# Kernel optimization log

Hardware: AMD Instinct MI355X
Metric: run time of the kernel (lower is better)

The kernel has to match this reference:

```python
import jax, jax.numpy as jnp
import numpy as np

B, T, NX, NY, E, BS = 2, 8, 32, 32, 768, 64
NB = E // BS            # 12 blocks
YM = NY // 2 + 1        # 17 rfft y modes
KM = 12                 # kept_modes (hardcoded in source)
XS = slice(YM - KM, YM + KM)  # slice(5,29) on the x-mode axis (faithful quirk: bounds use y_modes)
LAM = 0.01


def _ln(x, g, b, eps=1e-5):
    m = x.mean(-1, keepdims=True)
    v = ((x - m) ** 2).mean(-1, keepdims=True)
    return (x - m) / jnp.sqrt(v + eps) * g + b


def _softshrink(x, lam=LAM):
    return jnp.where(x > lam, x - lam, jnp.where(x < -lam, x + lam, jnp.zeros((), x.dtype)))


def setup_inputs() -> dict:
    key = jax.random.key(0)
    ks = jax.random.split(key, 8)
    s = 0.02
    return {
        'input': jax.random.normal(ks[0], (B, T, NX * NY, E), jnp.float32),
        'w1': s * jax.random.normal(ks[1], (2, NB, BS, BS), jnp.float32),
        'b1': s * jax.random.normal(ks[2], (2, 1, 1, 1, NB, BS), jnp.float32),
        'w2': s * jax.random.normal(ks[3], (2, NB, BS, BS), jnp.float32),
        'b2': s * jax.random.normal(ks[4], (2, 1, 1, 1, NB, BS), jnp.float32),
        'ln1_g': jnp.ones((E,), jnp.float32),
        'ln1_b': jnp.zeros((E,), jnp.float32),
        'ln2_g': jnp.ones((E,), jnp.float32),
        'ln2_b': jnp.zeros((E,), jnp.float32),
        'mw1': s * jax.random.normal(ks[5], (E, 4 * E), jnp.float32),
        'mb1': jnp.zeros((4 * E,), jnp.float32),
        'mw2': s * jax.random.normal(ks[6], (4 * E, E), jnp.float32),
        'mb2': jnp.zeros((E,), jnp.float32),
    }


def reference(input, w1, b1, w2, b2, ln1_g, ln1_b, ln2_g, ln2_b, mw1, mb1, mw2, mb2):
    residual = input
    h = _ln(input, ln1_g, ln1_b)                       # ln1
    r = h.reshape(B, T, NX, NY, E)
    fc = jnp.fft.rfft2(r, axes=(2, 3), norm='ortho')   # (B,T,NX,YM,E) complex
    fc = fc.reshape(B, T, NX, YM, NB, BS)
    fr = fc.real[:, :, XS, :KM]                        # (B,T,24,12,NB,BS)
    fi = fc.imag[:, :, XS, :KM]
    op = 'btxyni,nio->btxyno'
    o1r = jax.nn.gelu(jnp.einsum(op, fr, w1[0]) - jnp.einsum(op, fi, w1[1]) + b1[0], approximate=False)
    o1i = jax.nn.gelu(jnp.einsum(op, fi, w1[0]) + jnp.einsum(op, fr, w1[1]) + b1[1], approximate=False)
    o2r = jnp.einsum(op, o1r, w2[0]) - jnp.einsum(op, o1i, w2[1]) + b2[0]
    o2i = jnp.einsum(op, o1i, w2[0]) + jnp.einsum(op, o1r, w2[1]) + b2[1]
    out_r = jnp.zeros(fc.shape, jnp.float32).at[:, :, XS, :KM].set(_softshrink(o2r))
    out_i = jnp.zeros(fc.shape, jnp.float32).at[:, :, XS, :KM].set(_softshrink(o2i))
    oc = (out_r + 1j * out_i).reshape(B, T, NX, YM, E)
    spat = jnp.fft.irfft2(oc, s=(NX, NY), axes=(2, 3), norm='ortho').reshape(B, T, NX * NY, E)
    out = spat + h + residual                          # faithful: adds ln1(input) and original input
    res2 = out
    out = _ln(out, ln2_g, ln2_b)                       # ln2
    out = jax.nn.gelu(out @ mw1 + mb1, approximate=False) @ mw2 + mb2
    return out + res2
```

## Files before the change

kernel.cpp:

```cpp
#include <hip/hip_runtime.h>
#include <hip/hip_bf16.h>
#include <math.h>

typedef __bf16 bf16;
typedef __bf16 bf16x8 __attribute__((ext_vector_type(8)));
typedef float f32x4 __attribute__((ext_vector_type(4)));
typedef short short8 __attribute__((ext_vector_type(8)));

#define E_ 768
#define S_ 1024
#define BT_ 16
#define KM_ 12
#define KX_ 24
#define NPOS_ 4608
#define NB_ 12
#define TWOPI_32 0.19634954084936207740f

__device__ __forceinline__ float gelu_fast(float x) {
    float t = x * x;
    float u = x * fmaf(t, 0.0356774081f, 0.7978845608f);
    float e = __expf(2.0f * u);
    float th = fmaf(-2.0f, __fdividef(1.0f, e + 1.0f), 1.0f);
    float hx = 0.5f * x;
    return fmaf(hx, th, hx);
}

__device__ __forceinline__ bf16x8 neg8(bf16x8 v) {
    short8 s;
    __builtin_memcpy(&s, &v, 16);
    s ^= (short)0x8000;
    bf16x8 r;
    __builtin_memcpy(&r, &s, 16);
    return r;
}

__device__ __forceinline__ void gload16(bf16* lds, const bf16* g) {
    __builtin_amdgcn_global_load_lds(
        (const __attribute__((address_space(1))) void*)g,
        (__attribute__((address_space(3))) void*)lds,
        16, 0, 0);
}

__global__ __launch_bounds__(256) void k_ln_stats(const float* __restrict__ x,
                                                  float* __restrict__ mu, float* __restrict__ rs) {
    int w = threadIdx.x >> 6, l = threadIdx.x & 63;
    int row = blockIdx.x * 4 + w;
    const float4* p = (const float4*)(x + (size_t)row * E_ + l * 12);
    float4 a = p[0], b = p[1], c = p[2];
    float s  = a.x + a.y + a.z + a.w + b.x + b.y + b.z + b.w + c.x + c.y + c.z + c.w;
    float ss = a.x*a.x + a.y*a.y + a.z*a.z + a.w*a.w
             + b.x*b.x + b.y*b.y + b.z*b.z + b.w*b.w
             + c.x*c.x + c.y*c.y + c.z*c.z + c.w*c.w;
    #pragma unroll
    for (int off = 32; off > 0; off >>= 1) {
        s  += __shfl_xor(s, off);
        ss += __shfl_xor(ss, off);
    }
    if (l == 0) {
        float m = s * (1.0f / E_);
        float var = ss * (1.0f / E_) - m * m;
        mu[row] = m;
        rs[row] = rsqrtf(var + 1e-5f);
    }
}

__global__ __launch_bounds__(256) void k_ln2(const float* __restrict__ x,
                                             const float* __restrict__ g,
                                             const float* __restrict__ b,
                                             bf16* __restrict__ out) {
    int w = threadIdx.x >> 6, l = threadIdx.x & 63;
    int row = blockIdx.x * 4 + w;
    int e0 = l * 12;
    const float4* p = (const float4*)(x + (size_t)row * E_ + e0);
    float4 va = p[0], vb = p[1], vc = p[2];
    float v[12] = {va.x, va.y, va.z, va.w, vb.x, vb.y, vb.z, vb.w, vc.x, vc.y, vc.z, vc.w};
    float s = 0.f, ss = 0.f;
    #pragma unroll
    for (int j = 0; j < 12; j++) { s += v[j]; ss += v[j] * v[j]; }
    #pragma unroll
    for (int off = 32; off > 0; off >>= 1) {
        s  += __shfl_xor(s, off);
        ss += __shfl_xor(ss, off);
    }
    float m = s * (1.0f / E_);
    float var = ss * (1.0f / E_) - m * m;
    float r = rsqrtf(var + 1e-5f);
    const float4* gp = (const float4*)(g + e0);
    const float4* bp = (const float4*)(b + e0);
    float4 g0 = gp[0], g1 = gp[1], g2 = gp[2];
    float4 b0 = bp[0], b1 = bp[1], b2 = bp[2];
    float gg[12] = {g0.x, g0.y, g0.z, g0.w, g1.x, g1.y, g1.z, g1.w, g2.x, g2.y, g2.z, g2.w};
    float bbv[12] = {b0.x, b0.y, b0.z, b0.w, b1.x, b1.y, b1.z, b1.w, b2.x, b2.y, b2.z, b2.w};
    bf16 ov[12];
    #pragma unroll
    for (int j = 0; j < 12; j++) ov[j] = (bf16)((v[j] - m) * r * gg[j] + bbv[j]);
    bf16* op = out + (size_t)row * E_ + e0;
    *(uint2*)(op)     = *(uint2*)&ov[0];
    *(uint2*)(op + 4) = *(uint2*)&ov[4];
    *(uint2*)(op + 8) = *(uint2*)&ov[8];
}

__global__ __launch_bounds__(256) void k_dft_y(const float* __restrict__ inp,
                                               const float* __restrict__ mu, const float* __restrict__ rs,
                                               const float* __restrict__ g, const float* __restrict__ bb,
                                               float* __restrict__ gre, float* __restrict__ gim) {
    int bid = blockIdx.x;
    int ec = bid % 3, x = (bid / 3) % 32, bt = bid / 96;
    int t = threadIdx.x;
    int e = ec * 256 + t;
    float gv = g[e], bv = bb[e];
    int row0 = bt * S_ + x * 32;
    const float* base = inp + (size_t)row0 * E_ + e;
    float v[32];
    #pragma unroll
    for (int y = 0; y < 32; y++) {
        float m = mu[row0 + y], r = rs[row0 + y];
        v[y] = (base[(size_t)y * E_] - m) * r * gv + bv;
    }
    for (int ky = 0; ky < KM_; ky++) {
        float cK, sK;
        sincosf(TWOPI_32 * ky, &sK, &cK);
        float c = 1.f, s = 0.f, re = 0.f, ims = 0.f;
        #pragma unroll
        for (int y = 0; y < 32; y++) {
            re  = fmaf(v[y], c, re);
            ims = fmaf(v[y], s, ims);
            float cn = c * cK - s * sK;
            s = fmaf(s, cK, c * sK);
            c = cn;
        }
        size_t o = ((size_t)((bt * 32 + x) * KM_ + ky)) * E_ + e;
        gre[o] = re; gim[o] = -ims;
    }
}

__global__ __launch_bounds__(256) void k_dft_x(const float* __restrict__ gre, const float* __restrict__ gim,
                                               float* __restrict__ fr, float* __restrict__ fi) {
    int bid = blockIdx.x;
    int ec = bid % 3, ky = (bid / 3) % KM_, bt = bid / (3 * KM_);
    int t = threadIdx.x;
    int eo = ec * 256 + t;
    float gr[32], gi[32];
    #pragma unroll
    for (int x = 0; x < 32; x++) {
        size_t o = ((size_t)((bt * 32 + x) * KM_ + ky)) * E_ + eo;
        gr[x] = gre[o]; gi[x] = gim[o];
    }
    for (int kxi = 0; kxi < KX_; kxi++) {
        int kx = kxi + 5;
        float cK, sK;
        sincosf(TWOPI_32 * kx, &sK, &cK);
        float c = 1.f, s = 0.f, re = 0.f, im = 0.f;
        #pragma unroll
        for (int x = 0; x < 32; x++) {
            re = fmaf(gr[x], c, re);
            re = fmaf(gi[x], s, re);
            im = fmaf(gi[x], c, im);
            im = fmaf(-gr[x], s, im);
            float cn = c * cK - s * sK;
            s = fmaf(s, cK, c * sK);
            c = cn;
        }
        size_t p = (size_t)(bt * KX_ + kxi) * KM_ + ky;
        fr[p * E_ + eo] = re * (1.0f / 32.0f);
        fi[p * E_ + eo] = im * (1.0f / 32.0f);
    }
}

__global__ __launch_bounds__(256) void k_blockmlp(float* fr, float* fi,
                                                  const float* __restrict__ w1, const float* __restrict__ b1,
                                                  const float* __restrict__ w2, const float* __restrict__ b2) {
    int n = blockIdx.x / 36;
    int p0 = (blockIdx.x % 36) * 128;
    int t = threadIdx.x;
    __shared__ __align__(16) bf16 lXr[128 * 72];
    __shared__ __align__(16) bf16 lXi[128 * 72];
    __shared__ __align__(16) bf16 lW1a[64 * 72];
    __shared__ __align__(16) bf16 lW1b[64 * 72];
    __shared__ __align__(16) bf16 lW2a[64 * 72];
    __shared__ __align__(16) bf16 lW2b[64 * 72];

    {
        int o = t & 63, iq = t >> 6;
        const float* s1a = w1 + (size_t)n * 4096;
        const float* s1b = w1 + (size_t)(NB_ + n) * 4096;
        const float* s2a = w2 + (size_t)n * 4096;
        const float* s2b = w2 + (size_t)(NB_ + n) * 4096;
        #pragma unroll
        for (int ii = 0; ii < 16; ii++) {
            int i = iq * 16 + ii;
            lW1a[o * 72 + i] = (bf16)s1a[i * 64 + o];
            lW1b[o * 72 + i] = (bf16)s1b[i * 64 + o];
            lW2a[o * 72 + i] = (bf16)s2a[i * 64 + o];
            lW2b[o * 72 + i] = (bf16)s2b[i * 64 + o];
        }
    }
    {
        int ch4 = (t & 15) * 4, prow = t >> 4;
        #pragma unroll
        for (int rep = 0; rep < 8; rep++) {
            int p = rep * 16 + prow;
            size_t ga = (size_t)(p0 + p) * E_ + n * 64 + ch4;
            float4 vr = *(const float4*)&fr[ga];
            float4 vi = *(const float4*)&fi[ga];
            bf16 br[4] = {(bf16)vr.x, (bf16)vr.y, (bf16)vr.z, (bf16)vr.w};
            bf16 bi[4] = {(bf16)vi.x, (bf16)vi.y, (bf16)vi.z, (bf16)vi.w};
            *(uint2*)&lXr[p * 72 + ch4] = *(uint2*)br;
            *(uint2*)&lXi[p * 72 + ch4] = *(uint2*)bi;
        }
    }
    int w = t >> 6, l = t & 63, lr = l & 15, lq = l >> 4;
    float bias1r[4], bias1i[4], bias2r[4], bias2i[4];
    #pragma unroll
    for (int ni = 0; ni < 4; ni++) {
        int o = n * 64 + ni * 16 + lr;
        bias1r[ni] = b1[o]; bias1i[ni] = b1[NB_ * 64 + o];
        bias2r[ni] = b2[o]; bias2i[ni] = b2[NB_ * 64 + o];
    }
    __syncthreads();

    f32x4 a1r[2][4], a1i[2][4];
    #pragma unroll
    for (int mt = 0; mt < 2; mt++)
        #pragma unroll
        for (int ni = 0; ni < 4; ni++) { a1r[mt][ni] = (f32x4){0,0,0,0}; a1i[mt][ni] = (f32x4){0,0,0,0}; }
    #pragma unroll
    for (int ks = 0; ks < 2; ks++) {
        int k0 = ks * 32;
        bf16x8 xr[2], xi[2], xin[2];
        #pragma unroll
        for (int mt = 0; mt < 2; mt++) {
            int row = w * 32 + mt * 16 + lr;
            xr[mt]  = *(bf16x8*)&lXr[row * 72 + k0 + lq * 8];
            xi[mt]  = *(bf16x8*)&lXi[row * 72 + k0 + lq * 8];
            xin[mt] = neg8(xi[mt]);
        }
        #pragma unroll
        for (int ni = 0; ni < 4; ni++) {
            bf16x8 ba = *(bf16x8*)&lW1a[(ni * 16 + lr) * 72 + k0 + lq * 8];
            bf16x8 bb = *(bf16x8*)&lW1b[(ni * 16 + lr) * 72 + k0 + lq * 8];
            #pragma unroll
            for (int mt = 0; mt < 2; mt++) {
                a1r[mt][ni] = __builtin_amdgcn_mfma_f32_16x16x32_bf16(xr[mt],  ba, a1r[mt][ni], 0, 0, 0);
                a1r[mt][ni] = __builtin_amdgcn_mfma_f32_16x16x32_bf16(xin[mt], bb, a1r[mt][ni], 0, 0, 0);
                a1i[mt][ni] = __builtin_amdgcn_mfma_f32_16x16x32_bf16(xi[mt],  ba, a1i[mt][ni], 0, 0, 0);
                a1i[mt][ni] = __builtin_amdgcn_mfma_f32_16x16x32_bf16(xr[mt],  bb, a1i[mt][ni], 0, 0, 0);
            }
        }
    }
    #pragma unroll
    for (int mt = 0; mt < 2; mt++)
        #pragma unroll
        for (int ni = 0; ni < 4; ni++) {
            int o = ni * 16 + lr;
            #pragma unroll
            for (int r = 0; r < 4; r++) {
                int row = w * 32 + mt * 16 + lq * 4 + r;
                lXr[row * 72 + o] = (bf16)gelu_fast(a1r[mt][ni][r] + bias1r[ni]);
                lXi[row * 72 + o] = (bf16)gelu_fast(a1i[mt][ni][r] + bias1i[ni]);
            }
        }

    f32x4 a2r[2][4], a2i[2][4];
    #pragma unroll
    for (int mt = 0; mt < 2; mt++)
        #pragma unroll
        for (int ni = 0; ni < 4; ni++) { a2r[mt][ni] = (f32x4){0,0,0,0}; a2i[mt][ni] = (f32x4){0,0,0,0}; }
    #pragma unroll
    for (int ks = 0; ks < 2; ks++) {
        int k0 = ks * 32;
        bf16x8 xr[2], xi[2], xin[2];
        #pragma unroll
        for (int mt = 0; mt < 2; mt++) {
            int row = w * 32 + mt * 16 + lr;
            xr[mt]  = *(bf16x8*)&lXr[row * 72 + k0 + lq * 8];
            xi[mt]  = *(bf16x8*)&lXi[row * 72 + k0 + lq * 8];
            xin[mt] = neg8(xi[mt]);
        }
        #pragma unroll
        for (int ni = 0; ni < 4; ni++) {
            bf16x8 ba = *(bf16x8*)&lW2a[(ni * 16 + lr) * 72 + k0 + lq * 8];
            bf16x8 bb = *(bf16x8*)&lW2b[(ni * 16 + lr) * 72 + k0 + lq * 8];
            #pragma unroll
            for (int mt = 0; mt < 2; mt++) {
                a2r[mt][ni] = __builtin_amdgcn_mfma_f32_16x16x32_bf16(xr[mt],  ba, a2r[mt][ni], 0, 0, 0);
                a2r[mt][ni] = __builtin_amdgcn_mfma_f32_16x16x32_bf16(xin[mt], bb, a2r[mt][ni], 0, 0, 0);
                a2i[mt][ni] = __builtin_amdgcn_mfma_f32_16x16x32_bf16(xi[mt],  ba, a2i[mt][ni], 0, 0, 0);
                a2i[mt][ni] = __builtin_amdgcn_mfma_f32_16x16x32_bf16(xr[mt],  bb, a2i[mt][ni], 0, 0, 0);
            }
        }
    }
    #pragma unroll
    for (int mt = 0; mt < 2; mt++)
        #pragma unroll
        for (int ni = 0; ni < 4; ni++) {
            int o = ni * 16 + lr;
            #pragma unroll
            for (int r = 0; r < 4; r++) {
                int row = w * 32 + mt * 16 + lq * 4 + r;
                float vr = a2r[mt][ni][r] + bias2r[ni];
                float vi = a2i[mt][ni][r] + bias2i[ni];
                vr = (vr > 0.01f) ? vr - 0.01f : ((vr < -0.01f) ? vr + 0.01f : 0.0f);
                vi = (vi > 0.01f) ? vi - 0.01f : ((vi < -0.01f) ? vi + 0.01f : 0.0f);
                size_t ga = (size_t)(p0 + row) * E_ + n * 64 + o;
                fr[ga] = vr;
                fi[ga] = vi;
            }
        }
}

__global__ __launch_bounds__(256) void k_idft_x(const float* __restrict__ pr_, const float* __restrict__ pi_,
                                                float* __restrict__ zre, float* __restrict__ zim) {
    int bid = blockIdx.x;
    int ec = bid % 3, ky = (bid / 3) % KM_, bt = bid / (3 * KM_);
    int t = threadIdx.x;
    int eo = ec * 256 + t;
    float pr[KX_], pi[KX_];
    #pragma unroll
    for (int kxi = 0; kxi < KX_; kxi++) {
        size_t p = (size_t)(bt * KX_ + kxi) * KM_ + ky;
        pr[kxi] = pr_[p * E_ + eo];
        pi[kxi] = pi_[p * E_ + eo];
    }
    for (int x = 0; x < 32; x++) {
        float cX, sX, c, s;
        sincosf(TWOPI_32 * x, &sX, &cX);
        sincosf(TWOPI_32 * ((5 * x) & 31), &s, &c);
        float re = 0.f, im = 0.f;
        #pragma unroll
        for (int kxi = 0; kxi < KX_; kxi++) {
            re = fmaf(pr[kxi], c, re);
            re = fmaf(-pi[kxi], s, re);
            im = fmaf(pr[kxi], s, im);
            im = fmaf(pi[kxi], c, im);
            float cn = c * cX - s * sX;
            s = fmaf(s, cX, c * sX);
            c = cn;
        }
        size_t zo = ((size_t)((bt * 32 + x) * KM_ + ky)) * E_ + eo;
        zre[zo] = re; zim[zo] = im;
    }
}

__global__ __launch_bounds__(256) void k_idft_y_res(const float* __restrict__ zre, const float* __restrict__ zim,
                                                    const float* __restrict__ inp,
                                                    const float* __restrict__ mu, const float* __restrict__ rs,
                                                    const float* __restrict__ g, const float* __restrict__ bb,
                                                    float* __restrict__ out) {
    int bid = blockIdx.x;
    int ec = bid % 3, x = (bid / 3) % 32, bt = bid / 96;
    int t = threadIdx.x;
    int e = ec * 256 + t;
    float zr[KM_], zi[KM_];
    #pragma unroll
    for (int ky = 0; ky < KM_; ky++) {
        size_t zo = ((size_t)((bt * 32 + x) * KM_ + ky)) * E_ + e;
        zr[ky] = zre[zo];
        zi[ky] = zim[zo];
    }
    float gv = g[e], bv = bb[e];
    int row0 = bt * S_ + x * 32;
    for (int y = 0; y < 32; y++) {
        float cY, sY;
        sincosf(TWOPI_32 * y, &sY, &cY);
        float C = 2.f * cY, S = 2.f * sY;
        float v = zr[0];
        #pragma unroll
        for (int ky = 1; ky < KM_; ky++) {
            v = fmaf(zr[ky], C, v);
            v = fmaf(-zi[ky], S, v);
            float Cn = C * cY - S * sY;
            S = fmaf(S, cY, C * sY);
            C = Cn;
        }
        v *= (1.0f / 32.0f);
        size_t o = (size_t)(row0 + y) * E_ + e;
        float iv = inp[o];
        float m = mu[row0 + y], r = rs[row0 + y];
        out[o] = v + ((iv - m) * r * gv + bv) + iv;
    }
}

__global__ void k_transpose_cast(const float* __restrict__ src, bf16* __restrict__ dst, int R, int C) {
    __shared__ float tile[32][33];
    int c0 = blockIdx.x * 32, r0 = blockIdx.y * 32;
    int tx = threadIdx.x, ty = threadIdx.y;
    #pragma unroll
    for (int j = 0; j < 32; j += 8)
        tile[ty + j][tx] = src[(size_t)(r0 + ty + j) * C + c0 + tx];
    __syncthreads();
    #pragma unroll
    for (int j = 0; j < 32; j += 8)
        dst[(size_t)(c0 + ty + j) * R + r0 + tx] = (bf16)tile[tx][ty + j];
}

template<bool FUSE_GELU>
__global__ __launch_bounds__(512, 2) void k_gemm(const bf16* __restrict__ A, const bf16* __restrict__ Bt,
                                                 const float* __restrict__ bias, int M, int N, int K,
                                                 bf16* __restrict__ outb, float* __restrict__ outf) {
    __shared__ __align__(16) bf16 lA[2][256 * 64];
    __shared__ __align__(16) bf16 lB[2][256 * 64];
    int t = threadIdx.x;
    int m0 = blockIdx.x * 256, n0 = blockIdx.y * 256;
    int w = t >> 6, l = t & 63;
    int wm = (w >> 2) * 128, wn = (w & 3) * 64;
    int lr = l & 15, lq = l >> 4;
    int s0 = (lq ^ (lr & 7)) * 8;
    int s1 = s0 ^ 32;

    int sil  = w * 8 + (l >> 3);
    int gcol = ((l & 7) ^ ((l >> 3) & 7)) * 8;
    const bf16* pa = A  + (size_t)(m0 + sil) * K + gcol;
    const bf16* pb = Bt + (size_t)(n0 + sil) * K + gcol;
    int lofs = (w * 8) * 64;

    f32x4 acc[8][4];
    #pragma unroll
    for (int i = 0; i < 8; i++)
        #pragma unroll
        for (int j = 0; j < 4; j++)
            acc[i][j] = (f32x4){0.f, 0.f, 0.f, 0.f};

    int nk = K / 64;
#define STAGE_T(T, d) do { const size_t _ko = (size_t)(T) * 64;                  \
        gload16(&lA[d][lofs],            pa + _ko);                              \
        gload16(&lA[d][lofs + 4096],     pa + (size_t)64  * K + _ko);            \
        gload16(&lA[d][lofs + 8192],     pa + (size_t)128 * K + _ko);            \
        gload16(&lA[d][lofs + 12288],    pa + (size_t)192 * K + _ko);            \
        gload16(&lB[d][lofs],            pb + _ko);                              \
        gload16(&lB[d][lofs + 4096],     pb + (size_t)64  * K + _ko);            \
        gload16(&lB[d][lofs + 8192],     pb + (size_t)128 * K + _ko);            \
        gload16(&lB[d][lofs + 12288],    pb + (size_t)192 * K + _ko);            \
    } while (0)

    STAGE_T(0, 0);
    STAGE_T(1, 1);
    asm volatile("s_waitcnt vmcnt(8)" ::: "memory");
    __builtin_amdgcn_sched_barrier(0);
    __builtin_amdgcn_s_barrier();

    for (int kt = 0; kt < nk; kt++) {
        int d = kt & 1;
        bf16x8 a0[8], a1[8], b0[4], b1[4];
        #pragma unroll
        for (int ni = 0; ni < 4; ni++) {
            int ro = (wn + ni * 16 + lr) * 64;
            b0[ni] = *(bf16x8*)&lB[d][ro + s0];
            b1[ni] = *(bf16x8*)&lB[d][ro + s1];
        }
        #pragma unroll
        for (int mi = 0; mi < 8; mi++) {
            int ro = (wm + mi * 16 + lr) * 64;
            a0[mi] = *(bf16x8*)&lA[d][ro + s0];
            a1[mi] = *(bf16x8*)&lA[d][ro + s1];
        }
        __builtin_amdgcn_s_setprio(1);
        #pragma unroll
        for (int mi = 0; mi < 8; mi++)
            #pragma unroll
            for (int ni = 0; ni < 4; ni++)
                acc[mi][ni] = __builtin_amdgcn_mfma_f32_16x16x32_bf16(a0[mi], b0[ni], acc[mi][ni], 0, 0, 0);
        __builtin_amdgcn_s_setprio(0);
        asm volatile("s_waitcnt lgkmcnt(0)" ::: "memory");
        __builtin_amdgcn_sched_barrier(0);
        __builtin_amdgcn_s_barrier();

        if (kt + 2 < nk) STAGE_T(kt + 2, d);
        __builtin_amdgcn_s_setprio(1);
        #pragma unroll
        for (int mi = 0; mi < 8; mi++)
            #pragma unroll
            for (int ni = 0; ni < 4; ni++)
                acc[mi][ni] = __builtin_amdgcn_mfma_f32_16x16x32_bf16(a1[mi], b1[ni], acc[mi][ni], 0, 0, 0);
        __builtin_amdgcn_s_setprio(0);
        if (kt + 1 < nk) {
            if (kt + 2 < nk) asm volatile("s_waitcnt vmcnt(8)" ::: "memory");
            else             asm volatile("s_waitcnt vmcnt(0)" ::: "memory");
            __builtin_amdgcn_sched_barrier(0);
            __builtin_amdgcn_s_barrier();
        }
    }
#undef STAGE_T

    #pragma unroll
    for (int mi = 0; mi < 8; mi++) {
        #pragma unroll
        for (int ni = 0; ni < 4; ni++) {
            int col = n0 + wn + ni * 16 + lr;
            float bv = bias[col];
            #pragma unroll
            for (int r = 0; r < 4; r++) {
                int row = m0 + wm + mi * 16 + lq * 4 + r;
                float v = acc[mi][ni][r] + bv;
                if (FUSE_GELU) {
                    outb[(size_t)row * N + col] = (bf16)gelu_fast(v);
                } else {
                    size_t oo = (size_t)row * N + col;
                    outf[oo] = v + outf[oo];
                }
            }
        }
    }
}

extern "C" void kernel_launch(void* const* d_in, const int* in_sizes, int n_in,
                              void* d_out, int out_size, void* d_ws, size_t ws_size,
                              hipStream_t stream) {
    const float* input = (const float*)d_in[0];
    const float* w1    = (const float*)d_in[1];
    const float* b1    = (const float*)d_in[2];
    const float* w2    = (const float*)d_in[3];
    const float* b2    = (const float*)d_in[4];
    const float* ln1g  = (const float*)d_in[5];
    const float* ln1b  = (const float*)d_in[6];
    const float* ln2g  = (const float*)d_in[7];
    const float* ln2b  = (const float*)d_in[8];
    const float* mw1   = (const float*)d_in[9];
    const float* mb1   = (const float*)d_in[10];
    const float* mw2   = (const float*)d_in[11];
    const float* mb2   = (const float*)d_in[12];
    float* out = (float*)d_out;

    float* ws = (float*)d_ws;
    float* mu  = ws;
    float* rs  = ws + 16384;
    const size_t BASE = 32768;
    float* gre = ws + BASE;
    float* gim = gre + 4718592;
    float* fr  = ws + BASE + 2 * 4718592;
    float* fi  = fr + 3538944;
    bf16* lnA = (bf16*)(ws + BASE);
    bf16* w1T = (bf16*)(ws + BASE + 6291456);
    bf16* w2T = (bf16*)(ws + BASE + 7471104);
    bf16* mid = (bf16*)(ws + BASE + 8650752);

    const size_t fixed_fl = BASE + 6291456 + 1179648 + 1179648;
    size_t avail_fl = ws_size / 4;
    int nch;
    if      (avail_fl >= fixed_fl + 25165824) nch = 1;
    else if (avail_fl >= fixed_fl + 12582912) nch = 2;
    else                                      nch = 4;
    int MC = 16384 / nch;

    k_ln_stats<<<4096, 256, 0, stream>>>(input, mu, rs);
    k_dft_y<<<BT_ * 32 * 3, 256, 0, stream>>>(input, mu, rs, ln1g, ln1b, gre, gim);
    k_dft_x<<<BT_ * KM_ * 3, 256, 0, stream>>>(gre, gim, fr, fi);
    k_blockmlp<<<NB_ * 36, 256, 0, stream>>>(fr, fi, w1, b1, w2, b2);
    k_idft_x<<<BT_ * KM_ * 3, 256, 0, stream>>>(fr, fi, gre, gim);
    k_idft_y_res<<<BT_ * 32 * 3, 256, 0, stream>>>(gre, gim, input, mu, rs, ln1g, ln1b, out);
    k_ln2<<<4096, 256, 0, stream>>>(out, ln2g, ln2b, lnA);
    k_transpose_cast<<<dim3(3072 / 32, 768 / 32), dim3(32, 8), 0, stream>>>(mw1, w1T, 768, 3072);
    k_transpose_cast<<<dim3(768 / 32, 3072 / 32), dim3(32, 8), 0, stream>>>(mw2, w2T, 3072, 768);
    for (int c = 0; c < nch; c++) {
        const bf16* aC = lnA + (size_t)c * MC * 768;
        float* oC = out + (size_t)c * MC * 768;
        k_gemm<true><<<dim3(MC / 256, 12), 512, 0, stream>>>(aC, w1T, mb1, MC, 3072, 768, mid, nullptr);
        k_gemm<false><<<dim3(MC / 256, 3), 512, 0, stream>>>(mid, w2T, mb2, MC, 768, 3072, nullptr, oC);
    }
}
```

Before: 497.4 us.

## Restructure GEMM main loop into four-phase half-K pipeline with split LDS layout

Splits each 64-wide K tile in shared memory into two 32-wide halves with a new XOR swizzle. The main loop becomes four quarter phases, each reading a smaller set of A/B fragments and issuing one half-tile global prefetch between barriers. This interleaves global loads, LDS reads and MFMA work more finely and lowers the number of live fragment registers. In exchange it adds more barriers per iteration and relies on intricate vmcnt bookkeeping, so a mistake in the load ordering could cause hazards.

```diff
diff --git a/kernel.cpp b/kernel.cpp
--- a/kernel.cpp
+++ b/kernel.cpp
@@ -398,21 +398,21 @@
 __global__ __launch_bounds__(512, 2) void k_gemm(const bf16* __restrict__ A, const bf16* __restrict__ Bt,
                                                  const float* __restrict__ bias, int M, int N, int K,
                                                  bf16* __restrict__ outb, float* __restrict__ outf) {
-    __shared__ __align__(16) bf16 lA[2][256 * 64];
-    __shared__ __align__(16) bf16 lB[2][256 * 64];
+    __shared__ __align__(16) bf16 lA[2][2][256][32];
+    __shared__ __align__(16) bf16 lB[2][2][256][32];
     int t = threadIdx.x;
     int m0 = blockIdx.x * 256, n0 = blockIdx.y * 256;
     int w = t >> 6, l = t & 63;
     int wm = (w >> 2) * 128, wn = (w & 3) * 64;
     int lr = l & 15, lq = l >> 4;
-    int s0 = (lq ^ (lr & 7)) * 8;
-    int s1 = s0 ^ 32;
-
-    int sil  = w * 8 + (l >> 3);
-    int gcol = ((l & 7) ^ ((l >> 3) & 7)) * 8;
-    const bf16* pa = A  + (size_t)(m0 + sil) * K + gcol;
-    const bf16* pb = Bt + (size_t)(n0 + sil) * K + gcol;
-    int lofs = (w * 8) * 64;
+    int ps = (lq ^ (lr & 3)) * 8;
+
+    int srow = l >> 2;
+    int gsw  = (((l & 3) ^ ((l >> 2) & 3)) * 8);
+    const bf16* pa0 = A  + (size_t)(m0 + w * 16 + srow) * K + gsw;
+    const bf16* pa1 = pa0 + (size_t)128 * K;
+    const bf16* pb0 = Bt + (size_t)(n0 + w * 16 + srow) * K + gsw;
+    const bf16* pb1 = pb0 + (size_t)128 * K;
 
     f32x4 acc[8][4];
     #pragma unroll
@@ -422,65 +422,109 @@
             acc[i][j] = (f32x4){0.f, 0.f, 0.f, 0.f};
 
     int nk = K / 64;
-#define STAGE_T(T, d) do { const size_t _ko = (size_t)(T) * 64;                  \
-        gload16(&lA[d][lofs],            pa + _ko);                              \
-        gload16(&lA[d][lofs + 4096],     pa + (size_t)64  * K + _ko);            \
-        gload16(&lA[d][lofs + 8192],     pa + (size_t)128 * K + _ko);            \
-        gload16(&lA[d][lofs + 12288],    pa + (size_t)192 * K + _ko);            \
-        gload16(&lB[d][lofs],            pb + _ko);                              \
-        gload16(&lB[d][lofs + 4096],     pb + (size_t)64  * K + _ko);            \
-        gload16(&lB[d][lofs + 8192],     pb + (size_t)128 * K + _ko);            \
-        gload16(&lB[d][lofs + 12288],    pb + (size_t)192 * K + _ko);            \
-    } while (0)
-
-    STAGE_T(0, 0);
-    STAGE_T(1, 1);
-    asm volatile("s_waitcnt vmcnt(8)" ::: "memory");
+#define ST_A(T, ks, db) do { size_t _c = (size_t)(T) * 64 + (ks) * 32;   \
+        gload16(&lA[db][ks][w * 16][0],       pa0 + _c);                 \
+        gload16(&lA[db][ks][128 + w * 16][0], pa1 + _c); } while (0)
+#define ST_B(T, ks, db) do { size_t _c = (size_t)(T) * 64 + (ks) * 32;   \
+        gload16(&lB[db][ks][w * 16][0],       pb0 + _c);                 \
+        gload16(&lB[db][ks][128 + w * 16][0], pb1 + _c); } while (0)
+
+    ST_A(0, 0, 0); ST_B(0, 0, 0); ST_A(0, 1, 0); ST_B(0, 1, 0);
+    if (nk > 1) {
+        ST_B(1, 0, 1); ST_A(1, 0, 1); ST_B(1, 1, 1);
+        asm volatile("s_waitcnt vmcnt(6)" ::: "memory");
+    } else {
+        asm volatile("s_waitcnt vmcnt(0)" ::: "memory");
+    }
     __builtin_amdgcn_sched_barrier(0);
     __builtin_amdgcn_s_barrier();
-
+    __builtin_amdgcn_sched_barrier(0);
+
+    bf16x8 bA[4], bB[4];
     for (int kt = 0; kt < nk; kt++) {
         int d = kt & 1;
-        bf16x8 a0[8], a1[8], b0[4], b1[4];
-        #pragma unroll
-        for (int ni = 0; ni < 4; ni++) {
-            int ro = (wn + ni * 16 + lr) * 64;
-            b0[ni] = *(bf16x8*)&lB[d][ro + s0];
-            b1[ni] = *(bf16x8*)&lB[d][ro + s1];
-        }
-        #pragma unroll
-        for (int mi = 0; mi < 8; mi++) {
-            int ro = (wm + mi * 16 + lr) * 64;
-            a0[mi] = *(bf16x8*)&lA[d][ro + s0];
-            a1[mi] = *(bf16x8*)&lA[d][ro + s1];
-        }
-        __builtin_amdgcn_s_setprio(1);
-        #pragma unroll
-        for (int mi = 0; mi < 8; mi++)
-            #pragma unroll
-            for (int ni = 0; ni < 4; ni++)
-                acc[mi][ni] = __builtin_amdgcn_mfma_f32_16x16x32_bf16(a0[mi], b0[ni], acc[mi][ni], 0, 0, 0);
-        __builtin_amdgcn_s_setprio(0);
-        asm volatile("s_waitcnt lgkmcnt(0)" ::: "memory");
-        __builtin_amdgcn_sched_barrier(0);
-        __builtin_amdgcn_s_barrier();
-
-        if (kt + 2 < nk) STAGE_T(kt + 2, d);
-        __builtin_amdgcn_s_setprio(1);
-        #pragma unroll
-        for (int mi = 0; mi < 8; mi++)
-            #pragma unroll
-            for (int ni = 0; ni < 4; ni++)
-                acc[mi][ni] = __builtin_amdgcn_mfma_f32_16x16x32_bf16(a1[mi], b1[ni], acc[mi][ni], 0, 0, 0);
-        __builtin_amdgcn_s_setprio(0);
-        if (kt + 1 < nk) {
-            if (kt + 2 < nk) asm volatile("s_waitcnt vmcnt(8)" ::: "memory");
+        {
+            bf16x8 a[4];
+            #pragma unroll
+            for (int ni = 0; ni < 4; ni++) bA[ni] = *(bf16x8*)&lB[d][0][wn + ni * 16 + lr][ps];
+            #pragma unroll
+            for (int mi = 0; mi < 4; mi++) a[mi] = *(bf16x8*)&lA[d][0][wm + mi * 16 + lr][ps];
+            if (kt + 1 < nk) ST_A(kt + 1, 1, d ^ 1);
+            __builtin_amdgcn_s_barrier();
+            asm volatile("s_waitcnt lgkmcnt(0)" ::: "memory");
+            __builtin_amdgcn_sched_barrier(0);
+            __builtin_amdgcn_s_setprio(1);
+            #pragma unroll
+            for (int mi = 0; mi < 4; mi++)
+                #pragma unroll
+                for (int ni = 0; ni < 4; ni++)
+                    acc[mi][ni] = __builtin_amdgcn_mfma_f32_16x16x32_bf16(a[mi], bA[ni], acc[mi][ni], 0, 0, 0);
+            __builtin_amdgcn_s_setprio(0);
+            __builtin_amdgcn_s_barrier();
+            __builtin_amdgcn_sched_barrier(0);
+        }
+        {
+            bf16x8 a[4];
+            #pragma unroll
+            for (int ni = 0; ni < 4; ni++) bB[ni] = *(bf16x8*)&lB[d][1][wn + ni * 16 + lr][ps];
+            #pragma unroll
+            for (int mi = 0; mi < 4; mi++) a[mi] = *(bf16x8*)&lA[d][0][wm + 64 + mi * 16 + lr][ps];
+            if (kt + 2 < nk) ST_B(kt + 2, 0, d);
+            __builtin_amdgcn_s_barrier();
+            asm volatile("s_waitcnt lgkmcnt(0)" ::: "memory");
+            __builtin_amdgcn_sched_barrier(0);
+            __builtin_amdgcn_s_setprio(1);
+            #pragma unroll
+            for (int mi = 0; mi < 4; mi++)
+                #pragma unroll
+                for (int ni = 0; ni < 4; ni++)
+                    acc[4 + mi][ni] = __builtin_amdgcn_mfma_f32_16x16x32_bf16(a[mi], bA[ni], acc[4 + mi][ni], 0, 0, 0);
+            __builtin_amdgcn_s_setprio(0);
+            __builtin_amdgcn_s_barrier();
+            __builtin_amdgcn_sched_barrier(0);
+        }
+        {
+            bf16x8 a[4];
+            #pragma unroll
+            for (int mi = 0; mi < 4; mi++) a[mi] = *(bf16x8*)&lA[d][1][wm + mi * 16 + lr][ps];
+            if (kt + 2 < nk) ST_A(kt + 2, 0, d);
+            __builtin_amdgcn_s_barrier();
+            asm volatile("s_waitcnt lgkmcnt(0)" ::: "memory");
+            __builtin_amdgcn_sched_barrier(0);
+            __builtin_amdgcn_s_setprio(1);
+            #pragma unroll
+            for (int mi = 0; mi < 4; mi++)
+                #pragma unroll
+                for (int ni = 0; ni < 4; ni++)
+                    acc[mi][ni] = __builtin_amdgcn_mfma_f32_16x16x32_bf16(a[mi], bB[ni], acc[mi][ni], 0, 0, 0);
+            __builtin_amdgcn_s_setprio(0);
+            __builtin_amdgcn_s_barrier();
+            __builtin_amdgcn_sched_barrier(0);
+        }
+        {
+            bf16x8 a[4];
+            #pragma unroll
+            for (int mi = 0; mi < 4; mi++) a[mi] = *(bf16x8*)&lA[d][1][wm + 64 + mi * 16 + lr][ps];
+            if (kt + 2 < nk) ST_B(kt + 2, 1, d);
+            __builtin_amdgcn_s_barrier();
+            asm volatile("s_waitcnt lgkmcnt(0)" ::: "memory");
+            __builtin_amdgcn_sched_barrier(0);
+            __builtin_amdgcn_s_setprio(1);
+            #pragma unroll
+            for (int mi = 0; mi < 4; mi++)
+                #pragma unroll
+                for (int ni = 0; ni < 4; ni++)
+                    acc[4 + mi][ni] = __builtin_amdgcn_mfma_f32_16x16x32_bf16(a[mi], bB[ni], acc[4 + mi][ni], 0, 0, 0);
+            __builtin_amdgcn_s_setprio(0);
+            if (kt + 2 < nk) asm volatile("s_waitcnt vmcnt(6)" ::: "memory");
             else             asm volatile("s_waitcnt vmcnt(0)" ::: "memory");
             __builtin_amdgcn_sched_barrier(0);
             __builtin_amdgcn_s_barrier();
-        }
-    }
-#undef STAGE_T
+            __builtin_amdgcn_sched_barrier(0);
+        }
+    }
+#undef ST_A
+#undef ST_B
 
     #pragma unroll
     for (int mi = 0; mi < 8; mi++) {
```

Measured after the change: 523.1 us. 1.05x slower.
